# Kernel optimization log

Measured on AMD Instinct MI355X. Metric: run time of the kernel, lower is better.

Reference implementation:

```python
import jax, jax.numpy as jnp
import numpy as np

N_NODES = 100000


def _add_self_loops(edge_index, n):
    loop = jnp.arange(n, dtype=edge_index.dtype)
    src = jnp.concatenate([edge_index[0], loop])
    dst = jnp.concatenate([edge_index[1], loop])
    return src, dst


def _gcn_conv(x, src, dst, dinv_src, dinv_dst, W, b, n):
    # linear transform first (PyG GCNConv), then normalized scatter-add
    h = x @ W                                   # [N, out]
    msg = h[src] * (dinv_src * dinv_dst)[:, None]  # [E+N, out] gather
    out = jax.ops.segment_sum(msg, dst, num_segments=n)
    return out + b


def reference(x, edge_index, W0, b0, W1, b1, Wf, bf):
    n = N_NODES
    src, dst = _add_self_loops(edge_index, n)
    ones = jnp.ones(src.shape[0], dtype=x.dtype)
    deg = jax.ops.segment_sum(ones, dst, num_segments=n)
    dinv = jnp.where(deg > 0, jax.lax.rsqrt(jnp.maximum(deg, 1.0)), 0.0)
    dinv_src = dinv[src]
    dinv_dst = dinv[dst]

    h = jax.nn.relu(_gcn_conv(x, src, dst, dinv_src, dinv_dst, W0, b0, n))
    h = jax.nn.relu(_gcn_conv(h, src, dst, dinv_src, dinv_dst, W1, b1, n))
    return h @ Wf + bf


def setup_inputs() -> dict:
    key = jax.random.key(0)
    ks = jax.random.split(key, 8)
    n, e, f, h = N_NODES, 1600000, 32, 32
    return {
        "x": jax.random.normal(ks[0], (n, f), dtype=jnp.float32),
        "edge_index": jax.random.randint(ks[1], (2, e), 0, n, dtype=jnp.int64),
        "W0": jax.random.normal(ks[2], (f, h), dtype=jnp.float32) / np.sqrt(f),
        "b0": jnp.zeros((h,), dtype=jnp.float32),
        "W1": jax.random.normal(ks[3], (h, h), dtype=jnp.float32) / np.sqrt(h),
        "b1": jnp.zeros((h,), dtype=jnp.float32),
        "Wf": jax.random.normal(ks[4], (h, h), dtype=jnp.float32) / np.sqrt(h),
        "bf": jnp.zeros((h,), dtype=jnp.float32),
    }
```

## Files before the change

### kernel.cpp

```cpp
#include <hip/hip_runtime.h>
#include <hip/hip_fp16.h>


#define GNN_F 32
#define NBKT 391
#define BCAP 5120
#define CHUNK 8192

__global__ __launch_bounds__(256) void k_fused1(
    const float* __restrict__ x, const float* __restrict__ W0,
    __half* __restrict__ t,
    const int* __restrict__ src, const int* __restrict__ dst,
    int* bcnt, int* __restrict__ queue,
    int n, int e, int gemmBlocks) {
    __shared__ float Wl[32 * 32];
    __shared__ int hist[NBKT], curs[NBKT], base[NBKT];
    int tid = threadIdx.x;

    if (blockIdx.x < gemmBlocks) {
        ((float4*)Wl)[tid] = ((const float4*)W0)[tid];
        __syncthreads();
        int r = blockIdx.x * 256 + tid;
        if (r >= n) return;
        float xr[32];
        const float4* in4 = (const float4*)(x + (size_t)r * 32);
#pragma unroll
        for (int j = 0; j < 8; ++j) {
            float4 v = in4[j];
            xr[4 * j + 0] = v.x; xr[4 * j + 1] = v.y;
            xr[4 * j + 2] = v.z; xr[4 * j + 3] = v.w;
        }
        float acc[32];
#pragma unroll
        for (int c = 0; c < 32; ++c) acc[c] = 0.0f;
#pragma unroll
        for (int k = 0; k < 32; ++k) {
            float xv = xr[k];
#pragma unroll
            for (int c = 0; c < 32; ++c) acc[c] = fmaf(xv, Wl[k * 32 + c], acc[c]);
        }
        uint4* tp = (uint4*)(t + (size_t)r * 32);
#pragma unroll
        for (int j = 0; j < 4; ++j) {
            __half2 h0 = __floats2half2_rn(acc[8 * j + 0], acc[8 * j + 1]);
            __half2 h1 = __floats2half2_rn(acc[8 * j + 2], acc[8 * j + 3]);
            __half2 h2 = __floats2half2_rn(acc[8 * j + 4], acc[8 * j + 5]);
            __half2 h3 = __floats2half2_rn(acc[8 * j + 6], acc[8 * j + 7]);
            uint4 o;
            o.x = *(unsigned*)&h0; o.y = *(unsigned*)&h1;
            o.z = *(unsigned*)&h2; o.w = *(unsigned*)&h3;
            tp[j] = o;
        }
    } else {
        int c0 = (blockIdx.x - gemmBlocks) * CHUNK;
        int g0 = c0 >> 2;
        int n4 = e >> 2;
        for (int b = tid; b < NBKT; b += 256) hist[b] = 0;
        __syncthreads();
#pragma unroll
        for (int p = 0; p < CHUNK / 1024; ++p) {
            int g = g0 + p * 256 + tid;
            if (g < n4) {
                int4 d = ((const int4*)dst)[g];
                atomicAdd(&hist[((unsigned)d.x) >> 8], 1);
                atomicAdd(&hist[((unsigned)d.y) >> 8], 1);
                atomicAdd(&hist[((unsigned)d.z) >> 8], 1);
                atomicAdd(&hist[((unsigned)d.w) >> 8], 1);
            }
        }
        int tail0 = e & ~3;
        if (tail0 >= c0 && tail0 < c0 + CHUNK && tid < (e & 3))
            atomicAdd(&hist[((unsigned)dst[tail0 + tid]) >> 8], 1);
        __syncthreads();
        for (int b = tid; b < NBKT; b += 256) {
            int h = hist[b];
            base[b] = h ? atomicAdd(&bcnt[b], h) : 0;
            curs[b] = 0;
        }
        __syncthreads();
#pragma unroll
        for (int p = 0; p < CHUNK / 1024; ++p) {
            int g = g0 + p * 256 + tid;
            if (g < n4) {
                int4 d = ((const int4*)dst)[g];
                int4 sv = ((const int4*)src)[g];
                int b, l, slot;
                b = ((unsigned)d.x) >> 8; l = atomicAdd(&curs[b], 1); slot = base[b] + l;
                if (slot < BCAP) queue[(size_t)b * BCAP + slot] = (sv.x << 8) | (d.x & 255);
                b = ((unsigned)d.y) >> 8; l = atomicAdd(&curs[b], 1); slot = base[b] + l;
                if (slot < BCAP) queue[(size_t)b * BCAP + slot] = (sv.y << 8) | (d.y & 255);
                b = ((unsigned)d.z) >> 8; l = atomicAdd(&curs[b], 1); slot = base[b] + l;
                if (slot < BCAP) queue[(size_t)b * BCAP + slot] = (sv.z << 8) | (d.z & 255);
                b = ((unsigned)d.w) >> 8; l = atomicAdd(&curs[b], 1); slot = base[b] + l;
                if (slot < BCAP) queue[(size_t)b * BCAP + slot] = (sv.w << 8) | (d.w & 255);
            }
        }
        if (tail0 >= c0 && tail0 < c0 + CHUNK && tid < (e & 3)) {
            int j = tail0 + tid;
            int d = dst[j];
            int b = ((unsigned)d) >> 8;
            int l = atomicAdd(&curs[b], 1);
            int slot = base[b] + l;
            if (slot < BCAP) queue[(size_t)b * BCAP + slot] = (src[j] << 8) | (d & 255);
        }
    }
}

__global__ __launch_bounds__(512) void k_bscan(const int* __restrict__ bcnt,
                                               int* __restrict__ bbase,
                                               int* __restrict__ rs, int n) {
    __shared__ int sh[512];
    int t = threadIdx.x;
    int v = 0;
    if (t < NBKT) {
        v = bcnt[t];
        if (v > BCAP) v = BCAP;
    }
    sh[t] = v;
    __syncthreads();
    for (int off = 1; off < 512; off <<= 1) {
        int xv = (t >= off) ? sh[t - off] : 0;
        __syncthreads();
        sh[t] += xv;
        __syncthreads();
    }
    if (t < NBKT) bbase[t] = sh[t] - v;
    if (t == 511) rs[n] = sh[511];
}

__global__ __launch_bounds__(256) void k_build(
    const int* __restrict__ bcnt, const int* __restrict__ bbase,
    const int* __restrict__ queue,
    int* __restrict__ csr, int* __restrict__ rs, float* __restrict__ dinv,
    __half* __restrict__ t, int n) {
    __shared__ int hist[256], sh[256], cur[256];
    __shared__ float dsh[256];
    int b = blockIdx.x;
    int tid = threadIdx.x;
    int len = bcnt[b];
    if (len > BCAP) len = BCAP;
    const int* q = queue + (size_t)b * BCAP;

    hist[tid] = 0;
    __syncthreads();
    for (int i = tid; i < len; i += 256) atomicAdd(&hist[q[i] & 255], 1);
    __syncthreads();
    int c = hist[tid];
    sh[tid] = c;
    __syncthreads();
    for (int off = 1; off < 256; off <<= 1) {
        int xv = (tid >= off) ? sh[tid - off] : 0;
        __syncthreads();
        sh[tid] += xv;
        __syncthreads();
    }
    int myStart = bbase[b] + sh[tid] - c;
    int node = (b << 8) + tid;
    float dv = rsqrtf((float)(c + 1));
    if (node < n) {
        rs[node] = myStart;
        dinv[node] = dv;
    }
    dsh[tid] = dv;
    cur[tid] = myStart;
    __syncthreads();
    for (int i = tid; i < len; i += 256) {
        int qq = q[i];
        int p = atomicAdd(&cur[qq & 255], 1);
        csr[p] = ((unsigned)qq) >> 8;
    }
    int rows = n - (b << 8);
    if (rows > 256) rows = 256;
    uint4* t4 = (uint4*)(t + ((size_t)b << 8) * 32);
    for (int i = tid; i < rows * 4; i += 256) {
        float d = dsh[i >> 2];
        uint4 v = t4[i];
        __half2 h0 = *(__half2*)&v.x, h1 = *(__half2*)&v.y;
        __half2 h2 = *(__half2*)&v.z, h3 = *(__half2*)&v.w;
        float2 f0 = __half22float2(h0), f1 = __half22float2(h1);
        float2 f2 = __half22float2(h2), f3 = __half22float2(h3);
        h0 = __floats2half2_rn(f0.x * d, f0.y * d);
        h1 = __floats2half2_rn(f1.x * d, f1.y * d);
        h2 = __floats2half2_rn(f2.x * d, f2.y * d);
        h3 = __floats2half2_rn(f3.x * d, f3.y * d);
        v.x = *(unsigned*)&h0; v.y = *(unsigned*)&h1;
        v.z = *(unsigned*)&h2; v.w = *(unsigned*)&h3;
        t4[i] = v;
    }
}

__global__ __launch_bounds__(256) void k_gemm_h(
    const float* __restrict__ in,
    const float* __restrict__ W,
    const float* __restrict__ preb,
    const float* __restrict__ dscale,
    __half* __restrict__ t_out,
    int n) {
    __shared__ float Wl[32 * 32];
    __shared__ float pb[32];
    int tid = threadIdx.x;
    ((float4*)Wl)[tid] = ((const float4*)W)[tid];
    if (tid < 32) pb[tid] = preb[tid];
    __syncthreads();

    int r = blockIdx.x * 256 + tid;
    if (r >= n) return;

    float xr[32];
    const float4* in4 = (const float4*)(in + (size_t)r * 32);
#pragma unroll
    for (int j = 0; j < 8; ++j) {
        float4 v = in4[j];
        xr[4 * j + 0] = v.x; xr[4 * j + 1] = v.y;
        xr[4 * j + 2] = v.z; xr[4 * j + 3] = v.w;
    }
#pragma unroll
    for (int c = 0; c < 32; ++c) xr[c] = fmaxf(xr[c] + pb[c], 0.0f);

    float acc[32];
#pragma unroll
    for (int c = 0; c < 32; ++c) acc[c] = 0.0f;
#pragma unroll
    for (int k = 0; k < 32; ++k) {
        float xv = xr[k];
#pragma unroll
        for (int c = 0; c < 32; ++c) acc[c] = fmaf(xv, Wl[k * 32 + c], acc[c]);
    }
    float d = dscale[r];
#pragma unroll
    for (int c = 0; c < 32; ++c) acc[c] *= d;

    uint4* tp = (uint4*)(t_out + (size_t)r * 32);
#pragma unroll
    for (int j = 0; j < 4; ++j) {
        __half2 h0 = __floats2half2_rn(acc[8 * j + 0], acc[8 * j + 1]);
        __half2 h1 = __floats2half2_rn(acc[8 * j + 2], acc[8 * j + 3]);
        __half2 h2 = __floats2half2_rn(acc[8 * j + 4], acc[8 * j + 5]);
        __half2 h3 = __floats2half2_rn(acc[8 * j + 6], acc[8 * j + 7]);
        uint4 o;
        o.x = *(unsigned*)&h0; o.y = *(unsigned*)&h1;
        o.z = *(unsigned*)&h2; o.w = *(unsigned*)&h3;
        tp[j] = o;
    }
}

__global__ __launch_bounds__(256) void k_gemm_f(
    const float* __restrict__ in,
    const float* __restrict__ W,
    const float* __restrict__ preb,
    const float* __restrict__ postb,
    float* __restrict__ o_out,
    int n) {
    __shared__ float Wl[32 * 32];
    __shared__ float pb[32];
    int tid = threadIdx.x;
    ((float4*)Wl)[tid] = ((const float4*)W)[tid];
    if (tid < 32) pb[tid] = preb[tid];
    __syncthreads();

    int r = blockIdx.x * 256 + tid;
    if (r >= n) return;

    float xr[32];
    const float4* in4 = (const float4*)(in + (size_t)r * 32);
#pragma unroll
    for (int j = 0; j < 8; ++j) {
        float4 v = in4[j];
        xr[4 * j + 0] = v.x; xr[4 * j + 1] = v.y;
        xr[4 * j + 2] = v.z; xr[4 * j + 3] = v.w;
    }
#pragma unroll
    for (int c = 0; c < 32; ++c) xr[c] = fmaxf(xr[c] + pb[c], 0.0f);

    float acc[32];
#pragma unroll
    for (int c = 0; c < 32; ++c) acc[c] = postb[c];
#pragma unroll
    for (int k = 0; k < 32; ++k) {
        float xv = xr[k];
#pragma unroll
        for (int c = 0; c < 32; ++c) acc[c] = fmaf(xv, Wl[k * 32 + c], acc[c]);
    }

    float4* op = (float4*)(o_out + (size_t)r * 32);
#pragma unroll
    for (int j = 0; j < 8; ++j)
        op[j] = make_float4(acc[4 * j], acc[4 * j + 1], acc[4 * j + 2], acc[4 * j + 3]);
}

__global__ __launch_bounds__(256) void k_gather(
    const int* __restrict__ rs, const int* __restrict__ csr,
    const float* __restrict__ dinv, const __half* __restrict__ t,
    float* __restrict__ s, int n) {
    int idx = blockIdx.x * 256 + threadIdx.x;
    int row = idx >> 3;
    int j = idx & 7;
    if (row >= n) return;
    int e0 = rs[row];
    int e1 = rs[row + 1];
    float ax = 0.f, ay = 0.f, az = 0.f, aw = 0.f;
    int e = e0;
#define LOAD4(u, A, B)                                        \
    {                                                         \
        uint2 raw = ((const uint2*)(t + (size_t)(u) * 32))[j];\
        __half2 p0 = *(__half2*)&raw.x;                       \
        __half2 p1 = *(__half2*)&raw.y;                       \
        A = __half22float2(p0);                               \
        B = __half22float2(p1);                               \
    }
    for (; e + 7 < e1; e += 8) {
        int u0 = csr[e],     u1 = csr[e + 1], u2 = csr[e + 2], u3 = csr[e + 3];
        int u4 = csr[e + 4], u5 = csr[e + 5], u6 = csr[e + 6], u7 = csr[e + 7];
        float2 a0, b0, a1, b1, a2, b2, a3, b3, a4, b4, a5, b5, a6, b6, a7, b7;
        LOAD4(u0, a0, b0); LOAD4(u1, a1, b1); LOAD4(u2, a2, b2); LOAD4(u3, a3, b3);
        LOAD4(u4, a4, b4); LOAD4(u5, a5, b5); LOAD4(u6, a6, b6); LOAD4(u7, a7, b7);
        ax += ((a0.x + a1.x) + (a2.x + a3.x)) + ((a4.x + a5.x) + (a6.x + a7.x));
        ay += ((a0.y + a1.y) + (a2.y + a3.y)) + ((a4.y + a5.y) + (a6.y + a7.y));
        az += ((b0.x + b1.x) + (b2.x + b3.x)) + ((b4.x + b5.x) + (b6.x + b7.x));
        aw += ((b0.y + b1.y) + (b2.y + b3.y)) + ((b4.y + b5.y) + (b6.y + b7.y));
    }
    for (; e < e1; ++e) {
        int u = csr[e];
        float2 a, b;
        LOAD4(u, a, b);
        ax += a.x; ay += a.y; az += b.x; aw += b.y;
    }
    float2 sa, sb;
    LOAD4(row, sa, sb);
#undef LOAD4
    float d = dinv[row];
    float4 o;
    o.x = d * (ax + sa.x);
    o.y = d * (ay + sa.y);
    o.z = d * (az + sb.x);
    o.w = d * (aw + sb.y);
    ((float4*)(s + (size_t)row * 32))[j] = o;
}

extern "C" void kernel_launch(void* const* d_in, const int* in_sizes, int n_in,
                              void* d_out, int out_size, void* d_ws, size_t ws_size,
                              hipStream_t stream) {
    const float* x  = (const float*)d_in[0];
    const int*   ei = (const int*)d_in[1];
    const float* W0 = (const float*)d_in[2];
    const float* b0 = (const float*)d_in[3];
    const float* W1 = (const float*)d_in[4];
    const float* b1 = (const float*)d_in[5];
    const float* Wf = (const float*)d_in[6];
    const float* bf = (const float*)d_in[7];
    float* out = (float*)d_out;

    const int N = in_sizes[0] / GNN_F;
    const int E = in_sizes[1] / 2;
    const int* srcI = ei;
    const int* dstI = ei + E;

    const int gN = (N + 255) / 256;
    const int gG = (N * 8 + 255) / 256;
    const int nChunk = (E + CHUNK - 1) / CHUNK;

    char* ws = (char*)d_ws;
    size_t off = 0;
    auto alloc = [&](size_t bytes) {
        void* p = ws + off;
        off += (bytes + 127) & ~(size_t)127;
        return p;
    };
    int*    bcnt  = (int*)alloc((size_t)NBKT * 4);
    int*    bbase = (int*)alloc((size_t)NBKT * 4);
    int*    rs    = (int*)alloc((size_t)(N + 1) * 4);
    float*  dinv  = (float*)alloc((size_t)N * 4);
    int*    queue = (int*)alloc((size_t)NBKT * BCAP * 4);
    int*    csr   = (int*)alloc((size_t)E * 4);
    __half* t     = (__half*)alloc((size_t)N * GNN_F * 2);
    float*  s     = (float*)alloc((size_t)N * GNN_F * 4);
    (void)ws_size;

    hipMemsetAsync(bcnt, 0, (size_t)NBKT * 4, stream);

    k_fused1<<<gN + nChunk, 256, 0, stream>>>(x, W0, t, srcI, dstI, bcnt,
                                              queue, N, E, gN);
    k_bscan<<<1, 512, 0, stream>>>(bcnt, bbase, rs, N);
    k_build<<<NBKT, 256, 0, stream>>>(bcnt, bbase, queue, csr, rs, dinv, t, N);

    k_gather<<<gG, 256, 0, stream>>>(rs, csr, dinv, t, s, N);

    k_gemm_h<<<gN, 256, 0, stream>>>(s, W1, b0, dinv, t, N);
    k_gather<<<gG, 256, 0, stream>>>(rs, csr, dinv, t, s, N);

    k_gemm_f<<<gN, 256, 0, stream>>>(s, Wf, b1, bf, out, N);
}
```

Measured before the change: 200.6 us.

## Fuse gather with dense transform and fold bucket scan into CSR build

The separate bucket-scan kernel is removed. Each build block now computes its own bucket base by reducing the preceding bucket counts. The gather kernels are fused with the following 32x32 GEMM, bias and ReLU: each group of 8 threads stages its aggregated row in shared memory and multiplies it by W held in shared memory, writing the half-precision next-layer features or the final fp32 output directly. This removes the fp32 intermediate round trip through global memory and three kernel launches, at the cost of a redundant prefix sum per build block and an extra barrier plus shared-memory traffic in the gather kernels.

```diff
diff --git a/kernel.cpp b/kernel.cpp
--- a/kernel.cpp
+++ b/kernel.cpp
@@ -106,43 +106,35 @@
     }
 }
 
-__global__ __launch_bounds__(512) void k_bscan(const int* __restrict__ bcnt,
-                                               int* __restrict__ bbase,
-                                               int* __restrict__ rs, int n) {
-    __shared__ int sh[512];
-    int t = threadIdx.x;
-    int v = 0;
-    if (t < NBKT) {
-        v = bcnt[t];
-        if (v > BCAP) v = BCAP;
-    }
-    sh[t] = v;
-    __syncthreads();
-    for (int off = 1; off < 512; off <<= 1) {
-        int xv = (t >= off) ? sh[t - off] : 0;
-        __syncthreads();
-        sh[t] += xv;
-        __syncthreads();
-    }
-    if (t < NBKT) bbase[t] = sh[t] - v;
-    if (t == 511) rs[n] = sh[511];
-}
-
 __global__ __launch_bounds__(256) void k_build(
-    const int* __restrict__ bcnt, const int* __restrict__ bbase,
-    const int* __restrict__ queue,
+    const int* __restrict__ bcnt, const int* __restrict__ queue,
     int* __restrict__ csr, int* __restrict__ rs, float* __restrict__ dinv,
     __half* __restrict__ t, int n) {
+    __shared__ int red[256];
     __shared__ int hist[256], sh[256], cur[256];
     __shared__ float dsh[256];
     int b = blockIdx.x;
     int tid = threadIdx.x;
+
+    int part = 0;
+    for (int i = tid; i < b; i += 256) {
+        int v = bcnt[i];
+        part += (v > BCAP ? BCAP : v);
+    }
+    red[tid] = part;
+    hist[tid] = 0;
+    __syncthreads();
+#pragma unroll
+    for (int off = 128; off > 0; off >>= 1) {
+        if (tid < off) red[tid] += red[tid + off];
+        __syncthreads();
+    }
+    int bbase = red[0];
+
     int len = bcnt[b];
     if (len > BCAP) len = BCAP;
     const int* q = queue + (size_t)b * BCAP;
 
-    hist[tid] = 0;
-    __syncthreads();
     for (int i = tid; i < len; i += 256) atomicAdd(&hist[q[i] & 255], 1);
     __syncthreads();
     int c = hist[tid];
@@ -154,13 +146,14 @@
         sh[tid] += xv;
         __syncthreads();
     }
-    int myStart = bbase[b] + sh[tid] - c;
+    int myStart = bbase + sh[tid] - c;
     int node = (b << 8) + tid;
     float dv = rsqrtf((float)(c + 1));
     if (node < n) {
         rs[node] = myStart;
         dinv[node] = dv;
     }
+    if (b == (int)gridDim.x - 1 && tid == 255) rs[n] = myStart + c;
     dsh[tid] = dv;
     cur[tid] = myStart;
     __syncthreads();
@@ -171,6 +164,7 @@
     }
     int rows = n - (b << 8);
     if (rows > 256) rows = 256;
+    if (rows < 0) rows = 0;
     uint4* t4 = (uint4*)(t + ((size_t)b << 8) * 32);
     for (int i = tid; i < rows * 4; i += 256) {
         float d = dsh[i >> 2];
@@ -189,152 +183,110 @@
     }
 }
 
-__global__ __launch_bounds__(256) void k_gemm_h(
-    const float* __restrict__ in,
-    const float* __restrict__ W,
-    const float* __restrict__ preb,
-    const float* __restrict__ dscale,
-    __half* __restrict__ t_out,
-    int n) {
-    __shared__ float Wl[32 * 32];
-    __shared__ float pb[32];
-    int tid = threadIdx.x;
-    ((float4*)Wl)[tid] = ((const float4*)W)[tid];
-    if (tid < 32) pb[tid] = preb[tid];
-    __syncthreads();
-
-    int r = blockIdx.x * 256 + tid;
-    if (r >= n) return;
-
-    float xr[32];
-    const float4* in4 = (const float4*)(in + (size_t)r * 32);
-#pragma unroll
-    for (int j = 0; j < 8; ++j) {
-        float4 v = in4[j];
-        xr[4 * j + 0] = v.x; xr[4 * j + 1] = v.y;
-        xr[4 * j + 2] = v.z; xr[4 * j + 3] = v.w;
-    }
-#pragma unroll
-    for (int c = 0; c < 32; ++c) xr[c] = fmaxf(xr[c] + pb[c], 0.0f);
-
-    float acc[32];
-#pragma unroll
-    for (int c = 0; c < 32; ++c) acc[c] = 0.0f;
-#pragma unroll
-    for (int k = 0; k < 32; ++k) {
-        float xv = xr[k];
-#pragma unroll
-        for (int c = 0; c < 32; ++c) acc[c] = fmaf(xv, Wl[k * 32 + c], acc[c]);
-    }
-    float d = dscale[r];
-#pragma unroll
-    for (int c = 0; c < 32; ++c) acc[c] *= d;
-
-    uint4* tp = (uint4*)(t_out + (size_t)r * 32);
-#pragma unroll
-    for (int j = 0; j < 4; ++j) {
-        __half2 h0 = __floats2half2_rn(acc[8 * j + 0], acc[8 * j + 1]);
-        __half2 h1 = __floats2half2_rn(acc[8 * j + 2], acc[8 * j + 3]);
-        __half2 h2 = __floats2half2_rn(acc[8 * j + 4], acc[8 * j + 5]);
-        __half2 h3 = __floats2half2_rn(acc[8 * j + 6], acc[8 * j + 7]);
-        uint4 o;
-        o.x = *(unsigned*)&h0; o.y = *(unsigned*)&h1;
-        o.z = *(unsigned*)&h2; o.w = *(unsigned*)&h3;
-        tp[j] = o;
-    }
-}
-
-__global__ __launch_bounds__(256) void k_gemm_f(
-    const float* __restrict__ in,
-    const float* __restrict__ W,
-    const float* __restrict__ preb,
-    const float* __restrict__ postb,
-    float* __restrict__ o_out,
-    int n) {
-    __shared__ float Wl[32 * 32];
-    __shared__ float pb[32];
-    int tid = threadIdx.x;
-    ((float4*)Wl)[tid] = ((const float4*)W)[tid];
-    if (tid < 32) pb[tid] = preb[tid];
-    __syncthreads();
-
-    int r = blockIdx.x * 256 + tid;
-    if (r >= n) return;
-
-    float xr[32];
-    const float4* in4 = (const float4*)(in + (size_t)r * 32);
-#pragma unroll
-    for (int j = 0; j < 8; ++j) {
-        float4 v = in4[j];
-        xr[4 * j + 0] = v.x; xr[4 * j + 1] = v.y;
-        xr[4 * j + 2] = v.z; xr[4 * j + 3] = v.w;
-    }
-#pragma unroll
-    for (int c = 0; c < 32; ++c) xr[c] = fmaxf(xr[c] + pb[c], 0.0f);
-
-    float acc[32];
-#pragma unroll
-    for (int c = 0; c < 32; ++c) acc[c] = postb[c];
-#pragma unroll
-    for (int k = 0; k < 32; ++k) {
-        float xv = xr[k];
-#pragma unroll
-        for (int c = 0; c < 32; ++c) acc[c] = fmaf(xv, Wl[k * 32 + c], acc[c]);
-    }
-
-    float4* op = (float4*)(o_out + (size_t)r * 32);
-#pragma unroll
-    for (int j = 0; j < 8; ++j)
-        op[j] = make_float4(acc[4 * j], acc[4 * j + 1], acc[4 * j + 2], acc[4 * j + 3]);
-}
-
-__global__ __launch_bounds__(256) void k_gather(
+#define LOAD4(u, A, B)                                         \
+    {                                                          \
+        uint2 raw = ((const uint2*)(t + (size_t)(u) * 32))[j]; \
+        __half2 p0 = *(__half2*)&raw.x;                        \
+        __half2 p1 = *(__half2*)&raw.y;                        \
+        A = __half22float2(p0);                                \
+        B = __half22float2(p1);                                \
+    }
+
+#define GATHER_BODY()                                                          \
+    int idx = blockIdx.x * 256 + threadIdx.x;                                  \
+    int tid = threadIdx.x;                                                     \
+    int row = idx >> 3;                                                        \
+    bool live = row < n;                                                       \
+    if (!live) row = n - 1;                                                    \
+    int j = tid & 7;                                                           \
+    ((float4*)Wl)[tid] = ((const float4*)W)[tid];                              \
+    __syncthreads();                                                           \
+    int e0 = rs[row];                                                          \
+    int e1 = rs[row + 1];                                                      \
+    float ax = 0.f, ay = 0.f, az = 0.f, aw = 0.f;                              \
+    int e = e0;                                                                \
+    for (; e + 7 < e1; e += 8) {                                               \
+        int u0 = csr[e],     u1 = csr[e + 1], u2 = csr[e + 2], u3 = csr[e + 3];\
+        int u4 = csr[e + 4], u5 = csr[e + 5], u6 = csr[e + 6], u7 = csr[e + 7];\
+        float2 a0, b0v, a1, b1v, a2, b2v, a3, b3v;                             \
+        float2 a4, b4v, a5, b5v, a6, b6v, a7, b7v;                             \
+        LOAD4(u0, a0, b0v); LOAD4(u1, a1, b1v);                                \
+        LOAD4(u2, a2, b2v); LOAD4(u3, a3, b3v);                                \
+        LOAD4(u4, a4, b4v); LOAD4(u5, a5, b5v);                                \
+        LOAD4(u6, a6, b6v); LOAD4(u7, a7, b7v);                                \
+        ax += ((a0.x + a1.x) + (a2.x + a3.x)) + ((a4.x + a5.x) + (a6.x + a7.x));\
+        ay += ((a0.y + a1.y) + (a2.y + a3.y)) + ((a4.y + a5.y) + (a6.y + a7.y));\
+        az += ((b0v.x + b1v.x) + (b2v.x + b3v.x)) + ((b4v.x + b5v.x) + (b6v.x + b7v.x));\
+        aw += ((b0v.y + b1v.y) + (b2v.y + b3v.y)) + ((b4v.y + b5v.y) + (b6v.y + b7v.y));\
+    }                                                                          \
+    for (; e < e1; ++e) {                                                      \
+        int u = csr[e];                                                        \
+        float2 a, bb;                                                          \
+        LOAD4(u, a, bb);                                                       \
+        ax += a.x; ay += a.y; az += bb.x; aw += bb.y;                          \
+    }                                                                          \
+    float2 sa, sb;                                                             \
+    LOAD4(row, sa, sb);                                                        \
+    float d = dinv[row];                                                       \
+    float4 pb4 = ((const float4*)preb)[j];                                     \
+    float4 u4v;                                                                \
+    u4v.x = fmaxf(d * (ax + sa.x) + pb4.x, 0.0f);                              \
+    u4v.y = fmaxf(d * (ay + sa.y) + pb4.y, 0.0f);                              \
+    u4v.z = fmaxf(d * (az + sb.x) + pb4.z, 0.0f);                              \
+    u4v.w = fmaxf(d * (aw + sb.y) + pb4.w, 0.0f);                              \
+    int wv = tid >> 6;                                                         \
+    int g = (tid >> 3) & 7;                                                    \
+    float* urow = ur + wv * 320 + g * 40;                                      \
+    *(float4*)(urow + 4 * j) = u4v;                                            \
+    __syncthreads();
+
+__global__ __launch_bounds__(256) void k_gather_gemm(
     const int* __restrict__ rs, const int* __restrict__ csr,
     const float* __restrict__ dinv, const __half* __restrict__ t,
-    float* __restrict__ s, int n) {
-    int idx = blockIdx.x * 256 + threadIdx.x;
-    int row = idx >> 3;
-    int j = idx & 7;
-    if (row >= n) return;
-    int e0 = rs[row];
-    int e1 = rs[row + 1];
-    float ax = 0.f, ay = 0.f, az = 0.f, aw = 0.f;
-    int e = e0;
-#define LOAD4(u, A, B)                                        \
-    {                                                         \
-        uint2 raw = ((const uint2*)(t + (size_t)(u) * 32))[j];\
-        __half2 p0 = *(__half2*)&raw.x;                       \
-        __half2 p1 = *(__half2*)&raw.y;                       \
-        A = __half22float2(p0);                               \
-        B = __half22float2(p1);                               \
-    }
-    for (; e + 7 < e1; e += 8) {
-        int u0 = csr[e],     u1 = csr[e + 1], u2 = csr[e + 2], u3 = csr[e + 3];
-        int u4 = csr[e + 4], u5 = csr[e + 5], u6 = csr[e + 6], u7 = csr[e + 7];
-        float2 a0, b0, a1, b1, a2, b2, a3, b3, a4, b4, a5, b5, a6, b6, a7, b7;
-        LOAD4(u0, a0, b0); LOAD4(u1, a1, b1); LOAD4(u2, a2, b2); LOAD4(u3, a3, b3);
-        LOAD4(u4, a4, b4); LOAD4(u5, a5, b5); LOAD4(u6, a6, b6); LOAD4(u7, a7, b7);
-        ax += ((a0.x + a1.x) + (a2.x + a3.x)) + ((a4.x + a5.x) + (a6.x + a7.x));
-        ay += ((a0.y + a1.y) + (a2.y + a3.y)) + ((a4.y + a5.y) + (a6.y + a7.y));
-        az += ((b0.x + b1.x) + (b2.x + b3.x)) + ((b4.x + b5.x) + (b6.x + b7.x));
-        aw += ((b0.y + b1.y) + (b2.y + b3.y)) + ((b4.y + b5.y) + (b6.y + b7.y));
-    }
-    for (; e < e1; ++e) {
-        int u = csr[e];
-        float2 a, b;
-        LOAD4(u, a, b);
-        ax += a.x; ay += a.y; az += b.x; aw += b.y;
-    }
-    float2 sa, sb;
-    LOAD4(row, sa, sb);
-#undef LOAD4
-    float d = dinv[row];
-    float4 o;
-    o.x = d * (ax + sa.x);
-    o.y = d * (ay + sa.y);
-    o.z = d * (az + sb.x);
-    o.w = d * (aw + sb.y);
-    ((float4*)(s + (size_t)row * 32))[j] = o;
+    const float* __restrict__ W, const float* __restrict__ preb,
+    __half* __restrict__ t_out, int n) {
+    __shared__ float Wl[32 * 32];
+    __shared__ float ur[4 * 320];
+    GATHER_BODY()
+    float4 o = make_float4(0.f, 0.f, 0.f, 0.f);
+#pragma unroll
+    for (int k = 0; k < 32; ++k) {
+        float uk = urow[k];
+        float4 wv4 = ((const float4*)(Wl + k * 32))[j];
+        o.x = fmaf(uk, wv4.x, o.x);
+        o.y = fmaf(uk, wv4.y, o.y);
+        o.z = fmaf(uk, wv4.z, o.z);
+        o.w = fmaf(uk, wv4.w, o.w);
+    }
+    o.x *= d; o.y *= d; o.z *= d; o.w *= d;
+    if (live) {
+        __half2 h0 = __floats2half2_rn(o.x, o.y);
+        __half2 h1 = __floats2half2_rn(o.z, o.w);
+        uint2 pk;
+        pk.x = *(unsigned*)&h0; pk.y = *(unsigned*)&h1;
+        ((uint2*)(t_out + (size_t)row * 32))[j] = pk;
+    }
+}
+
+__global__ __launch_bounds__(256) void k_gather_out(
+    const int* __restrict__ rs, const int* __restrict__ csr,
+    const float* __restrict__ dinv, const __half* __restrict__ t,
+    const float* __restrict__ W, const float* __restrict__ preb,
+    const float* __restrict__ postb, float* __restrict__ out, int n) {
+    __shared__ float Wl[32 * 32];
+    __shared__ float ur[4 * 320];
+    GATHER_BODY()
+    float4 o = ((const float4*)postb)[j];
+#pragma unroll
+    for (int k = 0; k < 32; ++k) {
+        float uk = urow[k];
+        float4 wv4 = ((const float4*)(Wl + k * 32))[j];
+        o.x = fmaf(uk, wv4.x, o.x);
+        o.y = fmaf(uk, wv4.y, o.y);
+        o.z = fmaf(uk, wv4.z, o.z);
+        o.w = fmaf(uk, wv4.w, o.w);
+    }
+    if (live) ((float4*)(out + (size_t)row * 32))[j] = o;
 }
 
 extern "C" void kernel_launch(void* const* d_in, const int* in_sizes, int n_in,
@@ -367,26 +319,21 @@
         return p;
     };
     int*    bcnt  = (int*)alloc((size_t)NBKT * 4);
-    int*    bbase = (int*)alloc((size_t)NBKT * 4);
     int*    rs    = (int*)alloc((size_t)(N + 1) * 4);
     float*  dinv  = (float*)alloc((size_t)N * 4);
     int*    queue = (int*)alloc((size_t)NBKT * BCAP * 4);
     int*    csr   = (int*)alloc((size_t)E * 4);
-    __half* t     = (__half*)alloc((size_t)N * GNN_F * 2);
-    float*  s     = (float*)alloc((size_t)N * GNN_F * 4);
+    __half* t_a   = (__half*)alloc((size_t)N * GNN_F * 2);
+    __half* t_b   = (__half*)alloc((size_t)N * GNN_F * 2);
     (void)ws_size;
 
     hipMemsetAsync(bcnt, 0, (size_t)NBKT * 4, stream);
 
-    k_fused1<<<gN + nChunk, 256, 0, stream>>>(x, W0, t, srcI, dstI, bcnt,
+    k_fused1<<<gN + nChunk, 256, 0, stream>>>(x, W0, t_a, srcI, dstI, bcnt,
                                               queue, N, E, gN);
-    k_bscan<<<1, 512, 0, stream>>>(bcnt, bbase, rs, N);
-    k_build<<<NBKT, 256, 0, stream>>>(bcnt, bbase, queue, csr, rs, dinv, t, N);
-
-    k_gather<<<gG, 256, 0, stream>>>(rs, csr, dinv, t, s, N);
-
-    k_gemm_h<<<gN, 256, 0, stream>>>(s, W1, b0, dinv, t, N);
-    k_gather<<<gG, 256, 0, stream>>>(rs, csr, dinv, t, s, N);
-
-    k_gemm_f<<<gN, 256, 0, stream>>>(s, Wf, b1, bf, out, N);
-}
+    k_build<<<NBKT, 256, 0, stream>>>(bcnt, queue, csr, rs, dinv, t_a, N);
+
+    k_gather_gemm<<<gG, 256, 0, stream>>>(rs, csr, dinv, t_a, W1, b0, t_b, N);
+
+    k_gather_out<<<gG, 256, 0, stream>>>(rs, csr, dinv, t_b, Wf, b1, bf, out, N);
+}
```

New measurement: 174.4 us. 1.15x faster.
